# Kernel optimization log

Measured on AMD Instinct MI355X. Metric: run time of the kernel, lower is better.

## Reference

```python
import jax, jax.numpy as jnp
import numpy as np

# Tensor layout: x is [b, c, d, h, w, p, q, r] = [batch, channels, D, H, W, pd, ph, pw]
LETTERS = 'bcdhwpqr'

def axial_linear(x, W, b, axis, S, C):
    """LinearAlongDims1 over dims [1, axis]: jointly mixes channels and one
    spatial/patch axis. Torch flattens in (spatial, channel) order, so the
    (S*C, S*C) weight is reshaped to [S_out, C_out, S_in, C_in]."""
    a = LETTERS[axis]
    W4 = W.reshape(S, C, S, C)
    out_sub = LETTERS.replace('c', 'Y').replace(a, 'X')
    y = jnp.einsum(f'{LETTERS},XY{a}c->{out_sub}', x, W4)
    bshape = [1] * 8
    bshape[1] = C
    bshape[axis] = S
    return y + b.reshape(S, C).T.reshape(bshape)


def _make_linear_params(key, n):
    kw, kb = jax.random.split(key)
    bound = 1.0 / np.sqrt(n)
    W = jax.random.uniform(kw, (n, n), jnp.float32, -bound, bound)
    b = jax.random.uniform(kb, (n,), jnp.float32, -bound, bound)
    return W, b


def setup_inputs() -> dict:
    key = jax.random.key(0)
    ks = jax.random.split(key, 7)
    B, C, D, P = 2, 64, 16, 4
    x = jax.random.normal(ks[0], (B, C, D, D, D, P, P, P), jnp.float32)
    w_d, b_d = _make_linear_params(ks[1], C * D)      # image_d: dims [1,2]
    w_h, b_h = _make_linear_params(ks[2], C * D)      # image_h: dims [1,3]
    w_w, b_w = _make_linear_params(ks[3], C * D)      # image_w: dims [1,4]
    w_pd, b_pd = _make_linear_params(ks[4], C * P)    # patch_d: dims [1,5]
    w_ph, b_ph = _make_linear_params(ks[5], C * P)    # patch_h: dims [1,6]
    w_pw, b_pw = _make_linear_params(ks[6], C * P)    # patch_w: dims [1,7]
    return {
        'x': x,
        'w_d': w_d, 'b_d': b_d, 'w_h': w_h, 'b_h': b_h, 'w_w': w_w, 'b_w': b_w,
        'w_pd': w_pd, 'b_pd': b_pd, 'w_ph': w_ph, 'b_ph': b_ph,
        'w_pw': w_pw, 'b_pw': b_pw,
    }


def reference(x, w_d, b_d, w_h, b_h, w_w, b_w,
              w_pd, b_pd, w_ph, b_ph, w_pw, b_pw):
    C = x.shape[1]
    D = x.shape[2]
    P = x.shape[5]
    y = axial_linear(x, w_pd, b_pd, 5, P, C)
    y = y + axial_linear(x, w_ph, b_ph, 6, P, C)
    y = y + axial_linear(x, w_pw, b_pw, 7, P, C)
    y = y + axial_linear(x, w_d, b_d, 2, D, C)
    y = y + axial_linear(x, w_h, b_h, 3, D, C)
    y = y + axial_linear(x, w_w, b_w, 4, D, C)
    # shapes match -> leaky_relu + residual (module returns y; gn(x) is discarded)
    y = x + jax.nn.leaky_relu(y, negative_slope=0.01)
    return y
```

## Files before the change

kernel.cpp:

```cpp
#include <hip/hip_runtime.h>

typedef __attribute__((ext_vector_type(8))) short short8;
typedef __attribute__((ext_vector_type(4))) float floatx4;


__device__ __forceinline__ unsigned short f2bf(float f){
  unsigned int u = __float_as_uint(f);
  u += 0x7FFFu + ((u >> 16) & 1u);
  return (unsigned short)(u >> 16);
}

template<int AX>
__device__ __forceinline__ int tidx(int m, int a, int c){
  if      (AX==0){ int b=m>>14, t=m&16383;                         return (b<<24)|(c<<18)|(a<<14)|t; }
  else if (AX==1){ int b=m>>14, d=(m>>10)&15, t=m&1023;            return (b<<24)|(c<<18)|(d<<14)|(a<<10)|t; }
  else           { int b=m>>14, d=(m>>10)&15, h=(m>>6)&15, t=m&63; return (b<<24)|(c<<18)|(d<<14)|(h<<10)|(a<<6)|t; }
}

template<int AX>
__device__ __forceinline__ int srcbase(int m){
  if      (AX==0) return ((m>>14)<<24) | (((m>>10)&15)<<16) | (((m>>6)&15)<<12) | ((m&63)<<6);
  else if (AX==1) return ((m>>14)<<24) | (((m>>10)&15)<<20) | (((m>>6)&15)<<12) | ((m&63)<<6);
  else            return ((m>>14)<<24) | (((m>>10)&15)<<20) | (((m>>6)&15)<<16) | ((m&63)<<6);
}

#define ASYNC_CP16(g, l) \
  __builtin_amdgcn_global_load_lds( \
      (const __attribute__((address_space(1))) unsigned int*)(g), \
      (__attribute__((address_space(3))) unsigned int*)(l), 16, 0, 0)

__global__ __launch_bounds__(256) void castw_all(
    const float* __restrict__ wa, const float* __restrict__ wb, const float* __restrict__ wc,
    const float* __restrict__ wd_, const float* __restrict__ we, const float* __restrict__ wf,
    const float* __restrict__ bd_, const float* __restrict__ bh_, const float* __restrict__ bw_,
    const float* __restrict__ bpd_, const float* __restrict__ bph_, const float* __restrict__ bpw_,
    unsigned short* oa, unsigned short* ob, unsigned short* oc,
    unsigned short* od, unsigned short* oe, unsigned short* of_,
    float* __restrict__ Bimg, float* __restrict__ Bpat){
  int blk = blockIdx.x;
  if (blk < 6528){
    const float* src; unsigned short* dst; int idx;
    if (blk < 6144){ int wsel = blk >> 11, loc = blk & 2047;
      src = wsel==0?wa:(wsel==1?wb:wc); dst = wsel==0?oa:(wsel==1?ob:oc);
      idx = loc*256 + threadIdx.x; }
    else { int b2 = blk - 6144, wsel = b2 >> 7, loc = b2 & 127;
      src = wsel==0?wd_:(wsel==1?we:wf); dst = wsel==0?od:(wsel==1?oe:of_);
      idx = loc*256 + threadIdx.x; }
    float2 v = ((const float2*)src)[idx];
    ((unsigned int*)dst)[idx] = (unsigned int)f2bf(v.x) | ((unsigned int)f2bf(v.y) << 16);
  } else if (blk < 7552){
    int idx = (blk - 6528)*256 + threadIdx.x;
    int c = idx & 63, wv = (idx>>6)&15, hv = (idx>>10)&15, dv = idx>>14;
    Bimg[idx] = bd_[dv*64+c] + bh_[hv*64+c] + bw_[wv*64+c];
  } else {
    int idx = (blk - 7552)*256 + threadIdx.x;
    int c = idx & 63, tt = idx>>6;
    int p = tt>>4, q = (tt>>2)&3, r = tt&3;
    Bpat[idx] = bpd_[p*64+c] + bph_[q*64+c] + bpw_[r*64+c];
  }
}

__global__ __launch_bounds__(256) void transpose_cx(const float* __restrict__ x,
                                                    unsigned short* __restrict__ xt){
  __shared__ float T[64][65];
  int b  = blockIdx.x >> 12;
  int s0 = (blockIdx.x & 4095) * 64;
  int t = threadIdx.x;
  int cr = t >> 4, sq = t & 15;
  #pragma unroll
  for (int it = 0; it < 4; it++){
    int c = it*16 + cr;
    float4 v = *(const float4*)(x + (b<<24) + (c<<18) + s0 + sq*4);
    T[c][sq*4+0]=v.x; T[c][sq*4+1]=v.y; T[c][sq*4+2]=v.z; T[c][sq*4+3]=v.w;
  }
  __syncthreads();
  int sw = t >> 2, cq = t & 3;
  unsigned int pk[8];
  #pragma unroll
  for (int i=0;i<8;i++){
    float f0 = T[cq*16 + 2*i    ][sw];
    float f1 = T[cq*16 + 2*i + 1][sw];
    pk[i] = (unsigned int)f2bf(f0) | ((unsigned int)f2bf(f1) << 16);
  }
  uint4* dst = (uint4*)(xt + (b<<24) + ((s0 + sw)<<6) + cq*16);
  dst[0] = make_uint4(pk[0],pk[1],pk[2],pk[3]);
  dst[1] = make_uint4(pk[4],pk[5],pk[6],pk[7]);
}

template<int AXI, bool FIRST>
__device__ __forceinline__ void patch_axis(const unsigned short* Xs,
                                           const unsigned short* __restrict__ W,
                                           float* AccL, int w, int l16, int q8){
  floatx4 acc[4][2];
  #pragma unroll
  for (int nt=0;nt<4;nt++)
    #pragma unroll
    for (int mt=0;mt<2;mt++) acc[nt][mt] = (floatx4){0.f,0.f,0.f,0.f};

  #pragma unroll 2
  for (int kit = 0; kit < 8; kit++){
    int a = kit >> 1;
    short8 bf[2], af[4];
    int u = (AXI==0) ? (a*16 + l16)
          : (AXI==1) ? ((l16>>2)*16 + a*4 + (l16&3))
                     : ((l16>>2)*16 + (l16&3)*4 + a);
    int jg = ((kit & 1) << 2) + q8;
    #pragma unroll
    for (int mt = 0; mt < 2; mt++){
      int r = mt*64 + u;
      int j = jg ^ ((r ^ (r >> 3)) & 7);
      bf[mt] = *(const short8*)(Xs + r*64 + j*8);
    }
    #pragma unroll
    for (int nt = 0; nt < 4; nt++){
      int n = w*64 + nt*16 + l16;
      af[nt] = *(const short8*)(W + n*256 + kit*32 + q8*8);
    }
    #pragma unroll
    for (int nt=0; nt<4; nt++)
      #pragma unroll
      for (int mt=0; mt<2; mt++)
        acc[nt][mt] = __builtin_amdgcn_mfma_f32_16x16x32_bf16(af[nt], bf[mt], acc[nt][mt], 0,0,0);
  }

  int uo = (AXI==0) ? (w*16 + l16)
         : (AXI==1) ? ((l16>>2)*16 + w*4 + (l16&3))
                    : ((l16>>2)*16 + (l16&3)*4 + w);
  #pragma unroll
  for (int nt=0; nt<4; nt++)
    #pragma unroll
    for (int mt=0; mt<2; mt++){
      float* p = AccL + (mt*64 + uo)*65 + nt*16 + q8*4;
      #pragma unroll
      for (int rg=0; rg<4; rg++){
        if (FIRST) p[rg]  = acc[nt][mt][rg];
        else       p[rg] += acc[nt][mt][rg];
      }
    }
}

__global__ __launch_bounds__(256) void patch_fused(const unsigned short* __restrict__ xt,
    const unsigned short* __restrict__ Wp_, const unsigned short* __restrict__ Wq_,
    const unsigned short* __restrict__ Wr_, float* __restrict__ out){
  __shared__ float AccL[2*64*65];
  __shared__ unsigned short Xs[8192];
  int pp = blockIdx.x;
  int b = pp >> 11, dpair = pp & 2047;
  const unsigned short* xp = xt + (b<<24) + dpair*8192;
  int t = threadIdx.x, w = t>>6, lane = t&63, q8 = lane>>4, l16 = lane&15;

  #pragma unroll
  for (int i = 0; i < 4; i++){
    int L = i*256 + t;
    int r = L >> 3, jl = L & 7;
    int jg = jl ^ ((r ^ (r >> 3)) & 7);
    ASYNC_CP16(xp + r*64 + jg*8, Xs + i*2048 + w*512);
  }
  __syncthreads();

  patch_axis<0,true >(Xs, Wp_, AccL, w, l16, q8);
  __syncthreads();
  patch_axis<1,false>(Xs, Wq_, AccL, w, l16, q8);
  __syncthreads();
  patch_axis<2,false>(Xs, Wr_, AccL, w, l16, q8);
  __syncthreads();

  int sbase = dpair*128;
  #pragma unroll
  for (int it = 0; it < 32; it++){
    int lin = it*256 + t;
    int c = lin >> 7, rem = lin & 127, pt = rem >> 6, u = rem & 63;
    out[(b<<24) | (c<<18) | (sbase + pt*64 + u)] = AccL[(pt*64+u)*65 + c];
  }
}

#define WAITV8 asm volatile("s_waitcnt vmcnt(8)" ::: "memory")
#define WAITV0 asm volatile("s_waitcnt vmcnt(0)" ::: "memory")

template<int AX, int EPI>
__global__ __launch_bounds__(512, 2) void gemm_img(const unsigned short* __restrict__ xt,
                                                   const unsigned short* __restrict__ Wbf,
                                                   float* __restrict__ out,
                                                   const float* __restrict__ x,
                                                   const float* __restrict__ Bimg,
                                                   const float* __restrict__ Bpat){
  constexpr int K  = 1024;
  constexpr int SA = (AX==0)?(1<<20):(AX==1)?(1<<16):(1<<12);
  int bid = blockIdx.x;
  int mt = (bid >> 5) * 8 + (bid & 7);
  int nt = (bid >> 3) & 3;

  __shared__ unsigned short Xs0[256*64], Ws0[256*64];
  __shared__ unsigned short Xs1[256*64], Ws1[256*64];

  int t = threadIdx.x, lane = t & 63, wid = t >> 6;
  int wnb = (wid & 3) << 6;
  int wmb = (wid >> 2) << 7;
  int q8 = lane >> 4, l16 = lane & 15;

  floatx4 acc[4][8];
  #pragma unroll
  for (int i=0;i<4;i++)
    #pragma unroll
    for (int j=0;j<8;j++) acc[i][j] = (floatx4){0.f,0.f,0.f,0.f};

  const unsigned short* Wp = Wbf + (size_t)nt*256*K;

  int rr = t >> 3;
  int jg = (t & 7) ^ ((t >> 3) & 7);
  int baseX[4], baseWo[4];
  #pragma unroll
  for (int c=0;c<4;c++){
    int r = c*64 + rr;
    baseX[c]  = srcbase<AX>(mt*256 + r) + jg*8;
    baseWo[c] = r*K + jg*8;
  }

  int xoff[8], woff[4];
  #pragma unroll
  for (int j=0;j<8;j++){
    int rx = wmb + j*16 + l16; xoff[j] = rx*64 + ((q8 ^ (rx & 7)) << 3);
  }
  #pragma unroll
  for (int i=0;i<4;i++){
    int rw = wnb + i*16 + l16; woff[i] = rw*64 + ((q8 ^ (rw & 7)) << 3);
  }

  #define STAGE_T(a, XS, WS) do { \
    _Pragma("unroll") \
    for (int c=0;c<4;c++){ \
      ASYNC_CP16(xt + baseX[c] + (a)*SA, (XS) + c*4096 + wid*512); \
      ASYNC_CP16(Wp + baseWo[c] + (a)*64, (WS) + c*4096 + wid*512); \
    } } while(0)

  #define COMPUTE_T(XS, WS) do { \
    _Pragma("unroll") \
    for (int kk=0; kk<2; kk++){ \
      short8 wf[4], xf[8]; \
      _Pragma("unroll") \
      for (int i=0;i<4;i++) wf[i] = *(const short8*)&(WS)[woff[i] ^ (kk<<5)]; \
      _Pragma("unroll") \
      for (int j=0;j<8;j++) xf[j] = *(const short8*)&(XS)[xoff[j] ^ (kk<<5)]; \
      _Pragma("unroll") \
      for (int i=0;i<4;i++) \
        _Pragma("unroll") \
        for (int j=0;j<8;j++) \
          acc[i][j] = __builtin_amdgcn_mfma_f32_16x16x32_bf16(wf[i], xf[j], acc[i][j], 0,0,0); \
    } } while(0)

  STAGE_T(0, Xs0, Ws0);
  WAITV0;
  __builtin_amdgcn_s_barrier();
  STAGE_T(1, Xs1, Ws1);

  for (int a2 = 0; a2 < 8; a2++){
    COMPUTE_T(Xs0, Ws0);
    __builtin_amdgcn_s_barrier();
    if (a2 < 7){ STAGE_T(2*a2+2, Xs0, Ws0); WAITV8; }
    else       { WAITV0; }
    __builtin_amdgcn_s_barrier();
    COMPUTE_T(Xs1, Ws1);
    if (a2 < 7){
      __builtin_amdgcn_s_barrier();
      STAGE_T(2*a2+3, Xs1, Ws1);
      WAITV8;
      __builtin_amdgcn_s_barrier();
    }
  }
  #undef STAGE_T
  #undef COMPUTE_T

  #pragma unroll
  for (int i=0;i<4;i++){
    #pragma unroll
    for (int j=0;j<8;j++){
      int mg = mt*256 + wmb + j*16 + l16;
      if (EPI){
        int d = (mg>>10)&15, h = (mg>>6)&15, tt = mg&63;
        int n0 = nt*256 + wnb + i*16 + q8*4;
        int a = n0 >> 6, c0 = n0 & 63;
        float4 bi = *(const float4*)(Bimg + (((d*16 + h)*16 + a)*64 + c0));
        float4 bp = *(const float4*)(Bpat + (tt*64 + c0));
        float bs0 = bi.x + bp.x, bs1 = bi.y + bp.y, bs2 = bi.z + bp.z, bs3 = bi.w + bp.w;
        #pragma unroll
        for (int rg=0; rg<4; rg++){
          int ng = n0 + rg;
          int idx = tidx<AX>(mg, ng>>6, ng&63);
          float bsum = (rg==0)?bs0:(rg==1)?bs1:(rg==2)?bs2:bs3;
          float y = out[idx] + acc[i][j][rg] + bsum;
          out[idx] = x[idx] + (y >= 0.f ? y : 0.01f*y);
        }
      } else {
        #pragma unroll
        for (int rg=0; rg<4; rg++){
          int ng = nt*256 + wnb + i*16 + q8*4 + rg;
          int idx = tidx<AX>(mg, ng>>6, ng&63);
          out[idx] += acc[i][j][rg];
        }
      }
    }
  }
}

extern "C" void kernel_launch(void* const* d_in, const int* in_sizes, int n_in,
                              void* d_out, int out_size, void* d_ws, size_t ws_size,
                              hipStream_t stream){
  const float* x = (const float*)d_in[0];
  const float* Wsrc[6] = {(const float*)d_in[1], (const float*)d_in[3], (const float*)d_in[5],
                          (const float*)d_in[7], (const float*)d_in[9], (const float*)d_in[11]};
  const float* Bsrc[6] = {(const float*)d_in[2], (const float*)d_in[4], (const float*)d_in[6],
                          (const float*)d_in[8], (const float*)d_in[10], (const float*)d_in[12]};
  float* out = (float*)d_out;
  char* ws = (char*)d_ws;

  const size_t welems[6] = {1024u*1024u, 1024u*1024u, 1024u*1024u,
                            256u*256u, 256u*256u, 256u*256u};
  size_t wOff[6], o = 0;
  for (int i=0;i<6;i++){ wOff[i] = o; o += welems[i]*2; }
  size_t xtOff = (o + 255) & ~(size_t)255;
  size_t bimgOff = xtOff + ((size_t)1u<<25)*2;
  size_t bpatOff = bimgOff + (size_t)16*16*16*64*4;
  unsigned short* xt = (unsigned short*)(ws + xtOff);
  float* Bimg = (float*)(ws + bimgOff);
  float* Bpat = (float*)(ws + bpatOff);
  unsigned short* Wbf[6];
  for (int i=0;i<6;i++) Wbf[i] = (unsigned short*)(ws + wOff[i]);

  castw_all<<<7616,256,0,stream>>>(Wsrc[0],Wsrc[1],Wsrc[2],Wsrc[3],Wsrc[4],Wsrc[5],
                                   Bsrc[0],Bsrc[1],Bsrc[2],Bsrc[3],Bsrc[4],Bsrc[5],
                                   Wbf[0],Wbf[1],Wbf[2],Wbf[3],Wbf[4],Wbf[5],
                                   Bimg, Bpat);
  transpose_cx<<<8192,256,0,stream>>>(x, xt);

  patch_fused<<<4096,256,0,stream>>>(xt, Wbf[3], Wbf[4], Wbf[5], out);

  gemm_img<0,0><<<512,512,0,stream>>>(xt, Wbf[0], out, nullptr, nullptr, nullptr);
  gemm_img<1,0><<<512,512,0,stream>>>(xt, Wbf[1], out, nullptr, nullptr, nullptr);
  gemm_img<2,1><<<512,512,0,stream>>>(xt, Wbf[2], out, x, Bimg, Bpat);
}
```

Before: 853.2 us.

## Restructure double-buffer pipeline, prefetch patch weights, raise MFMA wave priority

The image GEMM loop now issues each async tile copy just before computing on the other buffer, then waits fully and syncs once per half-step. This replaces the earlier scheme of a barrier before staging plus a partial vmcnt wait, which was meant to cut barrier count and stalls. The patch-axis kernel register-double-buffers its global weight fragments one k-step ahead so global load latency overlaps the MFMAs. Both MFMA blocks are wrapped in s_setprio so the matrix work is favoured over other waves. The new schedule drops a barrier between finishing compute on a buffer and restaging it, so correctness rests on the barrier ordering, and the full vmcnt(0) waits may expose more load latency.

```diff
diff --git a/kernel.cpp b/kernel.cpp
--- a/kernel.cpp
+++ b/kernel.cpp
@@ -97,10 +97,25 @@
     #pragma unroll
     for (int mt=0;mt<2;mt++) acc[nt][mt] = (floatx4){0.f,0.f,0.f,0.f};
 
-  #pragma unroll 2
+  const unsigned short* Wn[4];
+  #pragma unroll
+  for (int nt = 0; nt < 4; nt++){
+    int n = w*64 + nt*16 + l16;
+    Wn[nt] = W + n*256 + q8*8;
+  }
+  short8 af[2][4];
+  #pragma unroll
+  for (int nt = 0; nt < 4; nt++) af[0][nt] = *(const short8*)(Wn[nt]);
+
+  #pragma unroll
   for (int kit = 0; kit < 8; kit++){
+    if (kit < 7){
+      #pragma unroll
+      for (int nt = 0; nt < 4; nt++)
+        af[(kit+1)&1][nt] = *(const short8*)(Wn[nt] + (kit+1)*32);
+    }
     int a = kit >> 1;
-    short8 bf[2], af[4];
+    short8 bf[2];
     int u = (AXI==0) ? (a*16 + l16)
           : (AXI==1) ? ((l16>>2)*16 + a*4 + (l16&3))
                      : ((l16>>2)*16 + (l16&3)*4 + a);
@@ -111,16 +126,13 @@
       int j = jg ^ ((r ^ (r >> 3)) & 7);
       bf[mt] = *(const short8*)(Xs + r*64 + j*8);
     }
-    #pragma unroll
-    for (int nt = 0; nt < 4; nt++){
-      int n = w*64 + nt*16 + l16;
-      af[nt] = *(const short8*)(W + n*256 + kit*32 + q8*8);
-    }
+    __builtin_amdgcn_s_setprio(1);
     #pragma unroll
     for (int nt=0; nt<4; nt++)
       #pragma unroll
       for (int mt=0; mt<2; mt++)
-        acc[nt][mt] = __builtin_amdgcn_mfma_f32_16x16x32_bf16(af[nt], bf[mt], acc[nt][mt], 0,0,0);
+        acc[nt][mt] = __builtin_amdgcn_mfma_f32_16x16x32_bf16(af[kit&1][nt], bf[mt], acc[nt][mt], 0,0,0);
+    __builtin_amdgcn_s_setprio(0);
   }
 
   int uo = (AXI==0) ? (w*16 + l16)
@@ -174,7 +186,6 @@
   }
 }
 
-#define WAITV8 asm volatile("s_waitcnt vmcnt(8)" ::: "memory")
 #define WAITV0 asm volatile("s_waitcnt vmcnt(0)" ::: "memory")
 
 template<int AX, int EPI>
@@ -241,29 +252,30 @@
       for (int i=0;i<4;i++) wf[i] = *(const short8*)&(WS)[woff[i] ^ (kk<<5)]; \
       _Pragma("unroll") \
       for (int j=0;j<8;j++) xf[j] = *(const short8*)&(XS)[xoff[j] ^ (kk<<5)]; \
+      __builtin_amdgcn_s_setprio(1); \
       _Pragma("unroll") \
       for (int i=0;i<4;i++) \
         _Pragma("unroll") \
         for (int j=0;j<8;j++) \
           acc[i][j] = __builtin_amdgcn_mfma_f32_16x16x32_bf16(wf[i], xf[j], acc[i][j], 0,0,0); \
+      __builtin_amdgcn_s_setprio(0); \
     } } while(0)
 
   STAGE_T(0, Xs0, Ws0);
   WAITV0;
   __builtin_amdgcn_s_barrier();
-  STAGE_T(1, Xs1, Ws1);
 
   for (int a2 = 0; a2 < 8; a2++){
+    STAGE_T(2*a2+1, Xs1, Ws1);
     COMPUTE_T(Xs0, Ws0);
+    WAITV0;
     __builtin_amdgcn_s_barrier();
-    if (a2 < 7){ STAGE_T(2*a2+2, Xs0, Ws0); WAITV8; }
-    else       { WAITV0; }
-    __builtin_amdgcn_s_barrier();
+    if (a2 < 7){
+      STAGE_T(2*a2+2, Xs0, Ws0);
+    }
     COMPUTE_T(Xs1, Ws1);
     if (a2 < 7){
-      __builtin_amdgcn_s_barrier();
-      STAGE_T(2*a2+3, Xs1, Ws1);
-      WAITV8;
+      WAITV0;
       __builtin_amdgcn_s_barrier();
     }
   }
```

Result: faster. 772.6 us (-9.4%).

## Replace fused patch kernel with three generic tiled GEMM launches per patch axis

Applied to the files above, without the earlier changes.

Drops the fused patch kernel, which accumulated three small patch-axis GEMMs in LDS. Each patch axis now runs through the generalized double-buffered image GEMM kernel with K=256 and its own index mapping, and the first launch writes the output directly. It also raises wave priority around the MFMA block with s_setprio. The aim is better LDS-staged reuse of the patch weights and more MFMA throughput. The cost is two extra kernel launches and two extra read-modify-write passes over the full fp32 output.

```diff
diff --git a/kernel.cpp b/kernel.cpp
--- a/kernel.cpp
+++ b/kernel.cpp
@@ -14,15 +14,32 @@
 __device__ __forceinline__ int tidx(int m, int a, int c){
   if      (AX==0){ int b=m>>14, t=m&16383;                         return (b<<24)|(c<<18)|(a<<14)|t; }
   else if (AX==1){ int b=m>>14, d=(m>>10)&15, t=m&1023;            return (b<<24)|(c<<18)|(d<<14)|(a<<10)|t; }
-  else           { int b=m>>14, d=(m>>10)&15, h=(m>>6)&15, t=m&63; return (b<<24)|(c<<18)|(d<<14)|(h<<10)|(a<<6)|t; }
+  else if (AX==2){ int b=m>>14, d=(m>>10)&15, h=(m>>6)&15, t=m&63; return (b<<24)|(c<<18)|(d<<14)|(h<<10)|(a<<6)|t; }
+  else {
+    int b=m>>16, d=(m>>12)&15, h=(m>>8)&15, w=(m>>4)&15, u1=(m>>2)&3, u0=m&3;
+    int base = (b<<24)|(c<<18)|(d<<14)|(h<<10)|(w<<6);
+    if      (AX==3) return base | (a<<4) | (u1<<2) | u0;
+    else if (AX==4) return base | (u1<<4) | (a<<2) | u0;
+    else            return base | (u1<<4) | (u0<<2) | a;
+  }
 }
 
 template<int AX>
 __device__ __forceinline__ int srcbase(int m){
   if      (AX==0) return ((m>>14)<<24) | (((m>>10)&15)<<16) | (((m>>6)&15)<<12) | ((m&63)<<6);
   else if (AX==1) return ((m>>14)<<24) | (((m>>10)&15)<<20) | (((m>>6)&15)<<12) | ((m&63)<<6);
-  else            return ((m>>14)<<24) | (((m>>10)&15)<<20) | (((m>>6)&15)<<16) | ((m&63)<<6);
-}
+  else if (AX==2) return ((m>>14)<<24) | (((m>>10)&15)<<20) | (((m>>6)&15)<<16) | ((m&63)<<6);
+  else {
+    int b=m>>16, d=(m>>12)&15, h=(m>>8)&15, w=(m>>4)&15, u1=(m>>2)&3, u0=m&3;
+    int base = (b<<24) | (d<<20) | (h<<16) | (w<<12);
+    if      (AX==3) return base | (u1<<8) | (u0<<6);
+    else if (AX==4) return base | (u1<<10) | (u0<<6);
+    else            return base | (u1<<10) | (u0<<8);
+  }
+}
+
+template<int AX> struct AxSA { static constexpr int v =
+  (AX==0)?(1<<20):(AX==1)?(1<<16):(AX==2)?(1<<12):(AX==3)?(1<<10):(AX==4)?(1<<8):(1<<6); };
 
 #define ASYNC_CP16(g, l) \
   __builtin_amdgcn_global_load_lds( \
@@ -87,108 +104,21 @@
   dst[1] = make_uint4(pk[4],pk[5],pk[6],pk[7]);
 }
 
-template<int AXI, bool FIRST>
-__device__ __forceinline__ void patch_axis(const unsigned short* Xs,
-                                           const unsigned short* __restrict__ W,
-                                           float* AccL, int w, int l16, int q8){
-  floatx4 acc[4][2];
-  #pragma unroll
-  for (int nt=0;nt<4;nt++)
-    #pragma unroll
-    for (int mt=0;mt<2;mt++) acc[nt][mt] = (floatx4){0.f,0.f,0.f,0.f};
-
-  #pragma unroll 2
-  for (int kit = 0; kit < 8; kit++){
-    int a = kit >> 1;
-    short8 bf[2], af[4];
-    int u = (AXI==0) ? (a*16 + l16)
-          : (AXI==1) ? ((l16>>2)*16 + a*4 + (l16&3))
-                     : ((l16>>2)*16 + (l16&3)*4 + a);
-    int jg = ((kit & 1) << 2) + q8;
-    #pragma unroll
-    for (int mt = 0; mt < 2; mt++){
-      int r = mt*64 + u;
-      int j = jg ^ ((r ^ (r >> 3)) & 7);
-      bf[mt] = *(const short8*)(Xs + r*64 + j*8);
-    }
-    #pragma unroll
-    for (int nt = 0; nt < 4; nt++){
-      int n = w*64 + nt*16 + l16;
-      af[nt] = *(const short8*)(W + n*256 + kit*32 + q8*8);
-    }
-    #pragma unroll
-    for (int nt=0; nt<4; nt++)
-      #pragma unroll
-      for (int mt=0; mt<2; mt++)
-        acc[nt][mt] = __builtin_amdgcn_mfma_f32_16x16x32_bf16(af[nt], bf[mt], acc[nt][mt], 0,0,0);
-  }
-
-  int uo = (AXI==0) ? (w*16 + l16)
-         : (AXI==1) ? ((l16>>2)*16 + w*4 + (l16&3))
-                    : ((l16>>2)*16 + (l16&3)*4 + w);
-  #pragma unroll
-  for (int nt=0; nt<4; nt++)
-    #pragma unroll
-    for (int mt=0; mt<2; mt++){
-      float* p = AccL + (mt*64 + uo)*65 + nt*16 + q8*4;
-      #pragma unroll
-      for (int rg=0; rg<4; rg++){
-        if (FIRST) p[rg]  = acc[nt][mt][rg];
-        else       p[rg] += acc[nt][mt][rg];
-      }
-    }
-}
-
-__global__ __launch_bounds__(256) void patch_fused(const unsigned short* __restrict__ xt,
-    const unsigned short* __restrict__ Wp_, const unsigned short* __restrict__ Wq_,
-    const unsigned short* __restrict__ Wr_, float* __restrict__ out){
-  __shared__ float AccL[2*64*65];
-  __shared__ unsigned short Xs[8192];
-  int pp = blockIdx.x;
-  int b = pp >> 11, dpair = pp & 2047;
-  const unsigned short* xp = xt + (b<<24) + dpair*8192;
-  int t = threadIdx.x, w = t>>6, lane = t&63, q8 = lane>>4, l16 = lane&15;
-
-  #pragma unroll
-  for (int i = 0; i < 4; i++){
-    int L = i*256 + t;
-    int r = L >> 3, jl = L & 7;
-    int jg = jl ^ ((r ^ (r >> 3)) & 7);
-    ASYNC_CP16(xp + r*64 + jg*8, Xs + i*2048 + w*512);
-  }
-  __syncthreads();
-
-  patch_axis<0,true >(Xs, Wp_, AccL, w, l16, q8);
-  __syncthreads();
-  patch_axis<1,false>(Xs, Wq_, AccL, w, l16, q8);
-  __syncthreads();
-  patch_axis<2,false>(Xs, Wr_, AccL, w, l16, q8);
-  __syncthreads();
-
-  int sbase = dpair*128;
-  #pragma unroll
-  for (int it = 0; it < 32; it++){
-    int lin = it*256 + t;
-    int c = lin >> 7, rem = lin & 127, pt = rem >> 6, u = rem & 63;
-    out[(b<<24) | (c<<18) | (sbase + pt*64 + u)] = AccL[(pt*64+u)*65 + c];
-  }
-}
-
 #define WAITV8 asm volatile("s_waitcnt vmcnt(8)" ::: "memory")
 #define WAITV0 asm volatile("s_waitcnt vmcnt(0)" ::: "memory")
 
-template<int AX, int EPI>
-__global__ __launch_bounds__(512, 2) void gemm_img(const unsigned short* __restrict__ xt,
-                                                   const unsigned short* __restrict__ Wbf,
-                                                   float* __restrict__ out,
-                                                   const float* __restrict__ x,
-                                                   const float* __restrict__ Bimg,
-                                                   const float* __restrict__ Bpat){
-  constexpr int K  = 1024;
-  constexpr int SA = (AX==0)?(1<<20):(AX==1)?(1<<16):(1<<12);
-  int bid = blockIdx.x;
-  int mt = (bid >> 5) * 8 + (bid & 7);
-  int nt = (bid >> 3) & 3;
+template<int AX, int EPI, int K>
+__global__ __launch_bounds__(512, 2) void gemm_ax(const unsigned short* __restrict__ xt,
+                                                  const unsigned short* __restrict__ Wbf,
+                                                  float* __restrict__ out,
+                                                  const float* __restrict__ x,
+                                                  const float* __restrict__ Bimg,
+                                                  const float* __restrict__ Bpat){
+  constexpr int SA = AxSA<AX>::v;
+  constexpr int NT = K / 64;
+  int bid = blockIdx.x, mt, nt;
+  if (AX < 3){ mt = (bid >> 5) * 8 + (bid & 7); nt = (bid >> 3) & 3; }
+  else       { mt = bid; nt = 0; }
 
   __shared__ unsigned short Xs0[256*64], Ws0[256*64];
   __shared__ unsigned short Xs1[256*64], Ws1[256*64];
@@ -241,11 +171,13 @@
       for (int i=0;i<4;i++) wf[i] = *(const short8*)&(WS)[woff[i] ^ (kk<<5)]; \
       _Pragma("unroll") \
       for (int j=0;j<8;j++) xf[j] = *(const short8*)&(XS)[xoff[j] ^ (kk<<5)]; \
+      __builtin_amdgcn_s_setprio(1); \
       _Pragma("unroll") \
       for (int i=0;i<4;i++) \
         _Pragma("unroll") \
         for (int j=0;j<8;j++) \
           acc[i][j] = __builtin_amdgcn_mfma_f32_16x16x32_bf16(wf[i], xf[j], acc[i][j], 0,0,0); \
+      __builtin_amdgcn_s_setprio(0); \
     } } while(0)
 
   STAGE_T(0, Xs0, Ws0);
@@ -253,14 +185,14 @@
   __builtin_amdgcn_s_barrier();
   STAGE_T(1, Xs1, Ws1);
 
-  for (int a2 = 0; a2 < 8; a2++){
+  for (int a2 = 0; a2 < NT/2; a2++){
     COMPUTE_T(Xs0, Ws0);
     __builtin_amdgcn_s_barrier();
-    if (a2 < 7){ STAGE_T(2*a2+2, Xs0, Ws0); WAITV8; }
-    else       { WAITV0; }
+    if (a2 < NT/2-1){ STAGE_T(2*a2+2, Xs0, Ws0); WAITV8; }
+    else            { WAITV0; }
     __builtin_amdgcn_s_barrier();
     COMPUTE_T(Xs1, Ws1);
-    if (a2 < 7){
+    if (a2 < NT/2-1){
       __builtin_amdgcn_s_barrier();
       STAGE_T(2*a2+3, Xs1, Ws1);
       WAITV8;
@@ -275,7 +207,7 @@
     #pragma unroll
     for (int j=0;j<8;j++){
       int mg = mt*256 + wmb + j*16 + l16;
-      if (EPI){
+      if (EPI == 1){
         int d = (mg>>10)&15, h = (mg>>6)&15, tt = mg&63;
         int n0 = nt*256 + wnb + i*16 + q8*4;
         int a = n0 >> 6, c0 = n0 & 63;
@@ -295,7 +227,8 @@
         for (int rg=0; rg<4; rg++){
           int ng = nt*256 + wnb + i*16 + q8*4 + rg;
           int idx = tidx<AX>(mg, ng>>6, ng&63);
-          out[idx] += acc[i][j][rg];
+          if (EPI == 2) out[idx]  = acc[i][j][rg];
+          else          out[idx] += acc[i][j][rg];
         }
       }
     }
@@ -332,9 +265,11 @@
                                    Bimg, Bpat);
   transpose_cx<<<8192,256,0,stream>>>(x, xt);
 
-  patch_fused<<<4096,256,0,stream>>>(xt, Wbf[3], Wbf[4], Wbf[5], out);
-
-  gemm_img<0,0><<<512,512,0,stream>>>(xt, Wbf[0], out, nullptr, nullptr, nullptr);
-  gemm_img<1,0><<<512,512,0,stream>>>(xt, Wbf[1], out, nullptr, nullptr, nullptr);
-  gemm_img<2,1><<<512,512,0,stream>>>(xt, Wbf[2], out, x, Bimg, Bpat);
-}
+  gemm_ax<3,2,256><<<512,512,0,stream>>>(xt, Wbf[3], out, nullptr, nullptr, nullptr);
+  gemm_ax<4,0,256><<<512,512,0,stream>>>(xt, Wbf[4], out, nullptr, nullptr, nullptr);
+  gemm_ax<5,0,256><<<512,512,0,stream>>>(xt, Wbf[5], out, nullptr, nullptr, nullptr);
+
+  gemm_ax<0,0,1024><<<512,512,0,stream>>>(xt, Wbf[0], out, nullptr, nullptr, nullptr);
+  gemm_ax<1,0,1024><<<512,512,0,stream>>>(xt, Wbf[1], out, nullptr, nullptr, nullptr);
+  gemm_ax<2,1,1024><<<512,512,0,stream>>>(xt, Wbf[2], out, x, Bimg, Bpat);
+}
```

New measurement: 832.8 us. 1.02x faster.
